# Performance work log

Measured on AMD Instinct MI355X. Metric: run time of the kernel, lower is better.

Reference implementation:

```python
import jax, jax.numpy as jnp
import numpy as np

N = 50000
E = 400000
R = 6
DIMS = (20, 256, 256, 512)


def setup_inputs() -> dict:
    key = jax.random.key(0)
    ks = jax.random.split(key, 16)
    inp = {
        "x": jax.random.normal(ks[0], (N, DIMS[0]), dtype=jnp.float32),
        "edge_index": jax.random.randint(ks[1], (2, E), 0, N, dtype=jnp.int64),
        "edge_type": jax.random.randint(ks[2], (E,), 0, R, dtype=jnp.int64),
    }
    # RGCN layer params: relation weights [R, in, out], root weight [in, out], bias [out]
    for li, (din, dout) in enumerate(zip(DIMS, DIMS[1:])):
        s = 1.0 / np.sqrt(din)
        inp[f"W{li}"] = jax.random.normal(ks[3 + 3 * li], (R, din, dout), dtype=jnp.float32) * s
        inp[f"root{li}"] = jax.random.normal(ks[4 + 3 * li], (din, dout), dtype=jnp.float32) * s
        inp[f"b{li}"] = jnp.zeros((dout,), dtype=jnp.float32)
    return inp


def _rgcn_layer(x, src, dst, etype, W, root, b):
    # Relation-specific transform of all nodes: [R, N, dout]
    h = jnp.einsum('ni,rio->rno', x, W)
    # Gather per-edge messages h[etype[e], src[e]] -> [E, dout]
    msgs = h[etype, src]
    # Mean-aggregate per (destination, relation) segment (PyG aggr='mean')
    seg = dst * R + etype  # [E]
    sums = jax.ops.segment_sum(msgs, seg, num_segments=N * R)          # [N*R, dout]
    cnt = jax.ops.segment_sum(jnp.ones((msgs.shape[0],), x.dtype), seg, num_segments=N * R)
    mean = sums / jnp.maximum(cnt, 1.0)[:, None]
    agg = mean.reshape(N, R, -1).sum(axis=1)  # sum over relations
    return agg + x @ root + b


def reference(x, edge_index, edge_type, W0, root0, b0, W1, root1, b1, W2, root2, b2):
    src, dst = edge_index[0], edge_index[1]  # messages flow source -> target
    params = ((W0, root0, b0), (W1, root1, b1), (W2, root2, b2))
    h = x
    for (W, root, b) in params:
        h = _rgcn_layer(h, src, dst, edge_type, W, root, b)
        h = jax.nn.relu(h)
    h = jnp.tanh(h)
    z = jnp.max(h, axis=0)          # graph-level max pool over nodes -> [latent]
    z = z / jnp.linalg.norm(z)      # normalized latent space
    return z[None, :]               # [1, latent]
```

## Files before the change

kernel.cpp:

```cpp
#include <hip/hip_runtime.h>

#define N_NODES 50000
#define N_EDGES 400000
#define N_REL 6
#define NSEG (N_NODES * N_REL)
#define NTILE ((N_NODES + 63) / 64)

#define SCAN_TILE 1024
#define SCAN_NB ((NSEG + SCAN_TILE - 1) / SCAN_TILE)

typedef float4 f4;
typedef short bf16x8 __attribute__((ext_vector_type(8)));
typedef float f32x4 __attribute__((ext_vector_type(4)));
typedef float f32x16 __attribute__((ext_vector_type(16)));
typedef int i32x8 __attribute__((ext_vector_type(8)));
typedef int i32x4 __attribute__((ext_vector_type(4)));

typedef __attribute__((address_space(1))) const void gvoid_t;
typedef __attribute__((address_space(3))) void lvoid_t;

__device__ __forceinline__ void gl_lds16(const void* g, void* l) {
    __builtin_amdgcn_global_load_lds((gvoid_t*)g, (lvoid_t*)l, 16, 0, 0);
}

__device__ __forceinline__ unsigned enc_f32(float f) {
    unsigned u = __float_as_uint(f);
    return (u & 0x80000000u) ? ~u : (u | 0x80000000u);
}
__device__ __forceinline__ float dec_f32(unsigned e) {
    return __uint_as_float((e & 0x80000000u) ? (e ^ 0x80000000u) : ~e);
}
__device__ __forceinline__ unsigned short bf16_rne(float x) {
    unsigned u = __float_as_uint(x);
    return (unsigned short)((u + 0x7FFFu + ((u >> 16) & 1u)) >> 16);
}
__device__ __forceinline__ unsigned fp8x4(float a0, float a1, float a2, float a3) {
    unsigned r = __builtin_amdgcn_cvt_pk_fp8_f32(a0, a1, 0, 0);
    r = __builtin_amdgcn_cvt_pk_fp8_f32(a2, a3, r, 1);
    return r;
}
__device__ __forceinline__ unsigned char fp8_1(float v) {
    return (unsigned char)(__builtin_amdgcn_cvt_pk_fp8_f32(v, v, 0, 0) & 0xFF);
}

#define SWZ(row, slot) ((size_t)(row) * 32 + (((slot) ^ (((row) >> 1) & 3)) * 8))

__global__ void count_seg(const int* __restrict__ ei, const int* __restrict__ et,
                          int* __restrict__ cnt) {
    int e = blockIdx.x * blockDim.x + threadIdx.x;
    if (e < N_EDGES) atomicAdd(&cnt[ei[N_EDGES + e] * N_REL + et[e]], 1);
}

__global__ void scan1(int* __restrict__ cnt, int* __restrict__ bsum) {
    __shared__ int sh[256];
    int t = threadIdx.x, b = blockIdx.x;
    int base = b * SCAN_TILE + t * 4;
    int v[4]; int s = 0;
    #pragma unroll
    for (int i = 0; i < 4; ++i) {
        v[i] = (base + i < NSEG) ? cnt[base + i] : 0;
        s += v[i];
    }
    sh[t] = s; __syncthreads();
    for (int o = 1; o < 256; o <<= 1) {
        int x = (t >= o) ? sh[t - o] : 0;
        __syncthreads();
        sh[t] += x;
        __syncthreads();
    }
    int run = sh[t] - s;
    #pragma unroll
    for (int i = 0; i < 4; ++i) {
        if (base + i < NSEG) cnt[base + i] = run;
        run += v[i];
    }
    if (t == 255) bsum[b] = sh[255];
}

__global__ void scan2(int* __restrict__ bsum) {
    __shared__ int sh[512];
    int t = threadIdx.x;
    int v = (t < SCAN_NB) ? bsum[t] : 0;
    sh[t] = v; __syncthreads();
    for (int o = 1; o < 512; o <<= 1) {
        int x = (t >= o) ? sh[t - o] : 0;
        __syncthreads();
        sh[t] += x;
        __syncthreads();
    }
    if (t < SCAN_NB) bsum[t] = sh[t] - v;
}

__global__ void scan3(const int* __restrict__ part, const int* __restrict__ bsum,
                      int* __restrict__ rowptr, int* __restrict__ fillptr) {
    int t = threadIdx.x, b = blockIdx.x;
    int base = b * SCAN_TILE + t * 4;
    int off = bsum[b];
    #pragma unroll
    for (int i = 0; i < 4; ++i) {
        if (base + i < NSEG) {
            int v = part[base + i] + off;
            rowptr[base + i] = v;
            fillptr[base + i] = v;
        }
    }
    if (b == 0 && t == 0) rowptr[NSEG] = N_EDGES;
}

__global__ void fill_edges(const int* __restrict__ ei, const int* __restrict__ et,
                           int* __restrict__ fillptr, int* __restrict__ esrc) {
    int e = blockIdx.x * blockDim.x + threadIdx.x;
    if (e < N_EDGES) {
        int seg = ei[N_EDGES + e] * N_REL + et[e];
        int p = atomicAdd(&fillptr[seg], 1);
        esrc[p] = ei[e];
    }
}

__global__ void rcp_kernel(const int* __restrict__ rowptr, float* __restrict__ rcp) {
    int s = blockIdx.x * blockDim.x + threadIdx.x;
    if (s < NSEG) {
        int c = rowptr[s + 1] - rowptr[s];
        rcp[s] = 1.0f / (float)(c > 1 ? c : 1);
    }
}

__global__ void prep_w0(const float* __restrict__ Wf, const float* __restrict__ rootW,
                        unsigned short* __restrict__ Wt,
                        int K1, int din, int dout, int KB) {
    int k = blockIdx.x;
    int n = blockIdx.y * 256 + threadIdx.x;
    if (n >= dout) return;
    float v = 0.f;
    if (k < K1) v = Wf[(size_t)k * dout + n];
    else if (k < K1 + din) v = rootW[(size_t)(k - K1) * dout + n];
    Wt[(size_t)n * KB + k] = bf16_rne(v);
}

__global__ void prep_wpk8(const float* __restrict__ Wf, const float* __restrict__ rootW,
                          unsigned char* __restrict__ Wpk, int K1, int dout) {
    int k = blockIdx.x;
    int ct = blockIdx.y;
    int nl = threadIdx.x;
    int col = ct * 256 + nl;
    float v = (k < K1) ? Wf[(size_t)k * dout + col]
                       : rootW[(size_t)(k - K1) * dout + col];
    v *= 16.0f;
    int p = k >> 6;
    Wpk[((size_t)(ct * 28 + p)) * 16384 + (size_t)nl * 64 + (k & 63)] = fp8_1(v);
}

__global__ void gather0(const float* __restrict__ x, const int* __restrict__ rowptr,
                        const int* __restrict__ esrc, const float* __restrict__ rcp,
                        unsigned short* __restrict__ Abf0) {
    int idx = blockIdx.x * blockDim.x + threadIdx.x;
    if (idx >= NSEG * 5) return;
    int s = idx / 5, q = idx - s * 5;
    float ax = 0.f, ay = 0.f, az = 0.f, aw = 0.f;
    int e0 = rowptr[s], e1 = rowptr[s + 1];
    for (int e = e0; e < e1; ++e) {
        const f4 u = *(const f4*)&x[(size_t)esrc[e] * 20 + q * 4];
        ax += u.x; ay += u.y; az += u.z; aw += u.w;
    }
    float sc = rcp[s];
    int node = s / N_REL, rel = s - node * N_REL;
    unsigned short* p = &Abf0[(size_t)node * 160 + rel * 20 + q * 4];
    unsigned o0 = bf16_rne(ax * sc) | ((unsigned)bf16_rne(ay * sc) << 16);
    unsigned o1 = bf16_rne(az * sc) | ((unsigned)bf16_rne(aw * sc) << 16);
    *(unsigned*)(p + 0) = o0;
    *(unsigned*)(p + 2) = o1;
}

__global__ void copyx0(const float* __restrict__ x, unsigned short* __restrict__ Abf0) {
    int t = blockIdx.x * blockDim.x + threadIdx.x;
    int n = t >> 5, d = t & 31;
    if (n >= N_NODES || d >= 20) return;
    Abf0[(size_t)n * 160 + 120 + d] = bf16_rne(x[(size_t)n * 20 + d]);
}

__global__ void gather_all8(const unsigned char* __restrict__ h8, const int* __restrict__ rowptr,
                            const int* __restrict__ esrc, const float* __restrict__ rcp,
                            unsigned char* __restrict__ Apk) {
    int t = blockIdx.x * blockDim.x + threadIdx.x;
    int sl = t >> 3;
    int q = t & 7;
    if (sl < NSEG) {
        int e0 = rowptr[sl], e1 = rowptr[sl + 1];
        float a[32];
        #pragma unroll
        for (int i = 0; i < 32; ++i) a[i] = 0.f;
        for (int e = e0; e < e1; ++e) {
            const unsigned char* hp = &h8[(size_t)esrc[e] * 256 + q * 32];
            #pragma unroll
            for (int c = 0; c < 2; ++c) {
                int4 v = *(const int4*)&hp[c * 16];
                const unsigned* pu = (const unsigned*)&v;
                #pragma unroll
                for (int j = 0; j < 4; ++j) {
                    unsigned u = pu[j];
                    a[c * 16 + j * 4 + 0] += __builtin_amdgcn_cvt_f32_fp8(u, 0);
                    a[c * 16 + j * 4 + 1] += __builtin_amdgcn_cvt_f32_fp8(u, 1);
                    a[c * 16 + j * 4 + 2] += __builtin_amdgcn_cvt_f32_fp8(u, 2);
                    a[c * 16 + j * 4 + 3] += __builtin_amdgcn_cvt_f32_fp8(u, 3);
                }
            }
        }
        float sc = rcp[sl];
        int node = sl / 6, rel = sl - node * 6;
        int rt = node >> 6, m = node & 63;
        int ks = rel * 8 + q;
        unsigned ow[8];
        #pragma unroll
        for (int i = 0; i < 8; ++i)
            ow[i] = fp8x4(a[4 * i] * sc, a[4 * i + 1] * sc, a[4 * i + 2] * sc, a[4 * i + 3] * sc);
        int p = ks >> 1, sp = ks & 1;
        unsigned char* dst = Apk + ((size_t)(rt * 28 + p)) * 4096 + (size_t)m * 64;
        int rot = (m >> 1) & 3;
        *(int4*)(dst + (((sp * 2 + 0 + rot) & 3) * 16)) = make_int4(ow[0], ow[1], ow[2], ow[3]);
        *(int4*)(dst + (((sp * 2 + 1 + rot) & 3) * 16)) = make_int4(ow[4], ow[5], ow[6], ow[7]);
    } else if (sl < NSEG + N_NODES) {
        int node = sl - NSEG;
        int rt = node >> 6, m = node & 63;
        const unsigned char* hp = &h8[(size_t)node * 256 + q * 32];
        int4 lo = *(const int4*)(hp + 0);
        int4 hi = *(const int4*)(hp + 16);
        int ks = 48 + q;
        int p = ks >> 1, sp = ks & 1;
        unsigned char* dst = Apk + ((size_t)(rt * 28 + p)) * 4096 + (size_t)m * 64;
        int rot = (m >> 1) & 3;
        *(int4*)(dst + (((sp * 2 + 0 + rot) & 3) * 16)) = lo;
        *(int4*)(dst + (((sp * 2 + 1 + rot) & 3) * 16)) = hi;
    }
}

__global__ __launch_bounds__(256)
void gemm_l0(const unsigned short* __restrict__ A, const unsigned short* __restrict__ Wt,
             const float* __restrict__ bias, unsigned char* __restrict__ outH8,
             int Ktot, int KB, int dout) {
    __shared__ unsigned short As[64 * 32];
    __shared__ unsigned short Bs[256 * 32];
    const int tid = threadIdx.x;
    const int col0 = blockIdx.x * 256;
    const int row0 = blockIdx.y * 64;
    const int w = tid >> 6, l = tid & 63;
    f32x4 acc[4][4] = {};

    for (int k0 = 0; k0 < Ktot; k0 += 32) {
        {
            int m = tid >> 2, slot = tid & 3;
            int4 v = {0, 0, 0, 0};
            int mg = row0 + m;
            if (mg < N_NODES) v = *(const int4*)&A[(size_t)mg * Ktot + k0 + slot * 8];
            *(int4*)&As[SWZ(m, slot)] = v;
        }
        {
            int nb = tid >> 2, slot = tid & 3;
            #pragma unroll
            for (int j = 0; j < 4; ++j) {
                int n = nb + j * 64;
                int4 v = *(const int4*)&Wt[(size_t)(col0 + n) * KB + k0 + slot * 8];
                *(int4*)&Bs[SWZ(n, slot)] = v;
            }
        }
        __syncthreads();
        bf16x8 af[4], bfr[4];
        #pragma unroll
        for (int rf = 0; rf < 4; ++rf)
            af[rf] = *(const bf16x8*)&As[SWZ(rf * 16 + (l & 15), l >> 4)];
        #pragma unroll
        for (int cf = 0; cf < 4; ++cf)
            bfr[cf] = *(const bf16x8*)&Bs[SWZ(w * 64 + cf * 16 + (l & 15), l >> 4)];
        #pragma unroll
        for (int cf = 0; cf < 4; ++cf)
            #pragma unroll
            for (int rf = 0; rf < 4; ++rf)
                acc[rf][cf] = __builtin_amdgcn_mfma_f32_16x16x32_bf16(
                    af[rf], bfr[cf], acc[rf][cf], 0, 0, 0);
        __syncthreads();
    }

    const int colbase = col0 + w * 64;
    #pragma unroll
    for (int cf = 0; cf < 4; ++cf) {
        int c = colbase + cf * 16 + (l & 15);
        float bb = bias[c];
        #pragma unroll
        for (int rf = 0; rf < 4; ++rf)
            #pragma unroll
            for (int i = 0; i < 4; ++i) {
                int m = row0 + rf * 16 + (l >> 4) * 4 + i;
                if (m < N_NODES) {
                    float v = fmaxf(acc[rf][cf][i] + bb, 0.f);
                    outH8[(size_t)m * dout + c] = fp8_1(v);
                }
            }
    }
}

__global__ __launch_bounds__(256, 3)
void gemm_mx(const unsigned char* __restrict__ Apk, const unsigned char* __restrict__ Wpk,
             const float* __restrict__ bias, unsigned char* __restrict__ outH8,
             unsigned* __restrict__ maxbuf, int dout, int fuse) {
    __shared__ __align__(16) unsigned char As[3][16384];
    __shared__ unsigned lmax[256];

    const int tid = threadIdx.x;
    const int w = tid >> 6, l = tid & 63;
    const int row0 = blockIdx.y * 64;
    const int bcol = blockIdx.x * 256;
    const int cg0 = bcol + w * 64;
    const int ctIdx = cg0 >> 8;
    const int nOff = cg0 & 255;

    f32x16 acc[2][2] = {};
    i32x8 aF[2];
    i32x4 bq[2][4];

    const unsigned char* aBlock = Apk + (size_t)blockIdx.y * 28 * 4096;
    const unsigned char* bLane = Wpk + (size_t)ctIdx * 28 * 16384
                               + (size_t)(nOff + (l & 31)) * 64 + (size_t)(l >> 5) * 32;

#define SB() __builtin_amdgcn_sched_barrier(0)

#define STAGE(g, buf) do {                                                   \
        _Pragma("unroll")                                                    \
        for (int i = 0; i < 4; ++i) {                                        \
            int c = w * 4 + i;                                               \
            gl_lds16(aBlock + (size_t)(g) * 16384 + (size_t)c * 1024 + l * 16, \
                     &As[buf][c * 1024]);                                    \
        }                                                                    \
    } while (0)

#define LOADB(p, s) do {                                                     \
        const unsigned char* _bp = bLane + (size_t)(p) * 16384;              \
        asm volatile("global_load_dwordx4 %0, %1, off"                       \
                     : "=&v"(bq[s][0]) : "v"(_bp));                          \
        asm volatile("global_load_dwordx4 %0, %1, off offset:16"             \
                     : "=&v"(bq[s][1]) : "v"(_bp));                          \
        asm volatile("global_load_dwordx4 %0, %1, off offset:2048"           \
                     : "=&v"(bq[s][2]) : "v"(_bp));                          \
        asm volatile("global_load_dwordx4 %0, %1, off offset:2064"           \
                     : "=&v"(bq[s][3]) : "v"(_bp));                          \
    } while (0)

#define READA(buf, q) do {                                                   \
        _Pragma("unroll")                                                    \
        for (int rf = 0; rf < 2; ++rf) {                                     \
            int mrow = rf * 32 + (l & 31);                                   \
            int rot = (mrow >> 1) & 3;                                       \
            int g = (l >> 5) * 2;                                            \
            const unsigned char* base = &As[buf][(q) * 4096 + (size_t)mrow * 64]; \
            i32x4 lo = *(const i32x4*)(base + (((g + 0 + rot) & 3) * 16));   \
            i32x4 hi = *(const i32x4*)(base + (((g + 1 + rot) & 3) * 16));   \
            i32x8 r;                                                         \
            r[0] = lo[0]; r[1] = lo[1]; r[2] = lo[2]; r[3] = lo[3];          \
            r[4] = hi[0]; r[5] = hi[1]; r[6] = hi[2]; r[7] = hi[3];          \
            aF[rf] = r;                                                      \
        }                                                                    \
    } while (0)

#define DOMFMA(s) do {                                                       \
        i32x8 Bq0, Bq1;                                                      \
        Bq0[0] = bq[s][0][0]; Bq0[1] = bq[s][0][1];                          \
        Bq0[2] = bq[s][0][2]; Bq0[3] = bq[s][0][3];                          \
        Bq0[4] = bq[s][1][0]; Bq0[5] = bq[s][1][1];                          \
        Bq0[6] = bq[s][1][2]; Bq0[7] = bq[s][1][3];                          \
        Bq1[0] = bq[s][2][0]; Bq1[1] = bq[s][2][1];                          \
        Bq1[2] = bq[s][2][2]; Bq1[3] = bq[s][2][3];                          \
        Bq1[4] = bq[s][3][0]; Bq1[5] = bq[s][3][1];                          \
        Bq1[6] = bq[s][3][2]; Bq1[7] = bq[s][3][3];                          \
        acc[0][0] = __builtin_amdgcn_mfma_scale_f32_32x32x64_f8f6f4(         \
            aF[0], Bq0, acc[0][0], 0, 0, 0, 127, 0, 123);                    \
        acc[1][0] = __builtin_amdgcn_mfma_scale_f32_32x32x64_f8f6f4(         \
            aF[1], Bq0, acc[1][0], 0, 0, 0, 127, 0, 123);                    \
        acc[0][1] = __builtin_amdgcn_mfma_scale_f32_32x32x64_f8f6f4(         \
            aF[0], Bq1, acc[0][1], 0, 0, 0, 127, 0, 123);                    \
        acc[1][1] = __builtin_amdgcn_mfma_scale_f32_32x32x64_f8f6f4(         \
            aF[1], Bq1, acc[1][1], 0, 0, 0, 127, 0, 123);                    \
    } while (0)

#define PHASE(buf, q, s, WN, p) do {                                         \
        READA(buf, q);                                                       \
        asm volatile("s_waitcnt vmcnt(" WN ")");                             \
        SB();                                                                \
        __builtin_amdgcn_s_setprio(1);                                       \
        DOMFMA(s);                                                           \
        __builtin_amdgcn_s_setprio(0);                                       \
        SB();                                                                \
        LOADB(p, s);                                                         \
        SB();                                                                \
    } while (0)

#define SSTEP(S, TW) do {                                                    \
        asm volatile("s_waitcnt vmcnt(" TW ")");                             \
        SB();                                                                \
        __builtin_amdgcn_s_barrier();                                        \
        SB();                                                                \
        PHASE((S) % 3, 0, 0, "8", 4 * (S) + 2 <= 27 ? 4 * (S) + 2 : 27);     \
        PHASE((S) % 3, 1, 1, "8", 4 * (S) + 3 <= 27 ? 4 * (S) + 3 : 27);     \
        PHASE((S) % 3, 2, 0, "4", 4 * (S) + 4 <= 27 ? 4 * (S) + 4 : 27);     \
        PHASE((S) % 3, 3, 1, "4", 4 * (S) + 5 <= 27 ? 4 * (S) + 5 : 27);     \
        STAGE((S) + 2 <= 6 ? (S) + 2 : 6, ((S) + 2) % 3);                    \
        SB();                                                                \
    } while (0)

    STAGE(0, 0);
    SB();
    LOADB(0, 0);
    LOADB(1, 1);
    SB();
    STAGE(1, 1);
    SB();

    SSTEP(0, "12");
    SSTEP(1, "20");
    SSTEP(2, "20");
    SSTEP(3, "20");
    SSTEP(4, "20");
    SSTEP(5, "20");
    SSTEP(6, "20");

#undef SSTEP
#undef PHASE
#undef DOMFMA
#undef READA
#undef LOADB
#undef STAGE
#undef SB

    if (!fuse) {
        #pragma unroll
        for (int cf = 0; cf < 2; ++cf) {
            int c = cg0 + cf * 32 + (l & 31);
            float bb = bias[c];
            #pragma unroll
            for (int rf = 0; rf < 2; ++rf)
                #pragma unroll
                for (int reg = 0; reg < 16; ++reg) {
                    int m = row0 + rf * 32 + (reg & 3) + 8 * (reg >> 2) + 4 * (l >> 5);
                    if (m < N_NODES) {
                        float v = fmaxf(acc[rf][cf][reg] + bb, 0.f);
                        outH8[(size_t)m * dout + c] = fp8_1(v);
                    }
                }
        }
    } else {
        lmax[tid] = 0u;
        __syncthreads();
        #pragma unroll
        for (int cf = 0; cf < 2; ++cf) {
            int c = cg0 + cf * 32 + (l & 31);
            float bb = bias[c];
            float mv = 0.f;
            bool any = false;
            #pragma unroll
            for (int rf = 0; rf < 2; ++rf)
                #pragma unroll
                for (int reg = 0; reg < 16; ++reg) {
                    int m = row0 + rf * 32 + (reg & 3) + 8 * (reg >> 2) + 4 * (l >> 5);
                    if (m < N_NODES) {
                        float v = acc[rf][cf][reg] + bb;
                        mv = any ? fmaxf(mv, v) : v;
                        any = true;
                    }
                }
            if (any) atomicMax(&lmax[c - bcol], enc_f32(mv));
        }
        __syncthreads();
        atomicMax(&maxbuf[bcol + tid], lmax[tid]);
    }
}

__global__ void finalize_kernel(const unsigned* __restrict__ maxbuf,
                                float* __restrict__ out) {
    __shared__ float red[8];
    int c = threadIdx.x;
    float v = dec_f32(maxbuf[c]);
    v = fmaxf(v, 0.0f);
    float t = tanhf(v);
    float s = t * t;
    #pragma unroll
    for (int o = 32; o > 0; o >>= 1) s += __shfl_down(s, o);
    int wid = c >> 6;
    if ((c & 63) == 0) red[wid] = s;
    __syncthreads();
    if (c < 8) {
        float wsum = red[c];
        #pragma unroll
        for (int o = 4; o > 0; o >>= 1) wsum += __shfl_down(wsum, o);
        if (c == 0) red[0] = wsum;
    }
    __syncthreads();
    float norm = sqrtf(red[0]);
    out[c] = t / norm;
}

static inline size_t align_up(size_t v, size_t a) { return (v + a - 1) / a * a; }

extern "C" void kernel_launch(void* const* d_in, const int* in_sizes, int n_in,
                              void* d_out, int out_size, void* d_ws, size_t ws_size,
                              hipStream_t stream) {
    const float* x  = (const float*)d_in[0];
    const int*   ei = (const int*)d_in[1];
    const int*   et = (const int*)d_in[2];
    const float* W0 = (const float*)d_in[3];
    const float* r0 = (const float*)d_in[4];
    const float* b0 = (const float*)d_in[5];
    const float* W1 = (const float*)d_in[6];
    const float* r1 = (const float*)d_in[7];
    const float* b1 = (const float*)d_in[8];
    const float* W2 = (const float*)d_in[9];
    const float* r2 = (const float*)d_in[10];
    const float* b2 = (const float*)d_in[11];
    float* out = (float*)d_out;

    char* ws = (char*)d_ws;
    size_t off = 0;
    int* cntpart = (int*)(ws + off); off = align_up(off + (size_t)NSEG * 4, 256);
    int* bsum = (int*)(ws + off);    off = align_up(off + 512 * 4, 256);
    int* rowptr = (int*)(ws + off);  off = align_up(off + (size_t)(NSEG + 1) * 4, 256);
    int* fillptr = (int*)(ws + off); off = align_up(off + (size_t)NSEG * 4, 256);
    int* esrc = (int*)(ws + off);    off = align_up(off + (size_t)N_EDGES * 4, 256);
    float* rcp = (float*)(ws + off); off = align_up(off + (size_t)NSEG * 4, 256);
    unsigned* maxbuf = (unsigned*)(ws + off); off = align_up(off + 512 * 4, 256);
    unsigned short* Wt0 = (unsigned short*)(ws + off); off = align_up(off + (size_t)256 * 160 * 2, 256);
    unsigned char* Wpk1 = (unsigned char*)(ws + off); off = align_up(off + (size_t)1 * 28 * 16384, 256);
    unsigned char* Wpk2 = (unsigned char*)(ws + off); off = align_up(off + (size_t)2 * 28 * 16384, 256);
    unsigned char* hbuf1 = (unsigned char*)(ws + off); off = align_up(off + (size_t)N_NODES * 256, 256);
    unsigned char* hbuf2 = (unsigned char*)(ws + off); off = align_up(off + (size_t)N_NODES * 256, 256);
    unsigned short* Abf0 = (unsigned short*)(ws + off); off = align_up(off + (size_t)N_NODES * 160 * 2, 256);
    unsigned char* Apk = (unsigned char*)(ws + off); off = align_up(off + (size_t)NTILE * 28 * 4096, 256);
    if (ws_size < off) return;

    hipMemsetAsync(cntpart, 0, (size_t)NSEG * 4, stream);
    count_seg<<<(N_EDGES + 255) / 256, 256, 0, stream>>>(ei, et, cntpart);
    scan1<<<SCAN_NB, 256, 0, stream>>>(cntpart, bsum);
    scan2<<<1, 512, 0, stream>>>(bsum);
    scan3<<<SCAN_NB, 256, 0, stream>>>(cntpart, bsum, rowptr, fillptr);
    rcp_kernel<<<(NSEG + 255) / 256, 256, 0, stream>>>(rowptr, rcp);
    fill_edges<<<(N_EDGES + 255) / 256, 256, 0, stream>>>(ei, et, fillptr, esrc);
    hipMemsetAsync(maxbuf, 0, 512 * 4, stream);

    prep_w0<<<dim3(160, 1), 256, 0, stream>>>(W0, r0, Wt0, 120, 20, 256, 160);
    prep_wpk8<<<dim3(1792, 1), 256, 0, stream>>>(W1, r1, Wpk1, 1536, 256);
    prep_wpk8<<<dim3(1792, 2), 256, 0, stream>>>(W2, r2, Wpk2, 1536, 512);

    hipMemsetAsync(Abf0, 0, (size_t)N_NODES * 160 * 2, stream);
    gather0<<<(NSEG * 5 + 255) / 256, 256, 0, stream>>>(x, rowptr, esrc, rcp, Abf0);
    copyx0<<<(N_NODES * 32 + 255) / 256, 256, 0, stream>>>(x, Abf0);
    gemm_l0<<<dim3(1, NTILE), 256, 0, stream>>>(Abf0, Wt0, b0, hbuf1, 160, 160, 256);

    const int gthreads = (NSEG + N_NODES) * 8;

    gather_all8<<<(gthreads + 255) / 256, 256, 0, stream>>>(hbuf1, rowptr, esrc, rcp, Apk);
    gemm_mx<<<dim3(1, NTILE), 256, 0, stream>>>(Apk, Wpk1, b1, hbuf2, nullptr, 256, 0);

    gather_all8<<<(gthreads + 255) / 256, 256, 0, stream>>>(hbuf2, rowptr, esrc, rcp, Apk);
    gemm_mx<<<dim3(2, NTILE), 256, 0, stream>>>(Apk, Wpk2, b2, nullptr, maxbuf, 512, 1);

    finalize_kernel<<<1, 512, 0, stream>>>(maxbuf, out);
}
```

Measured before the change: 308.3 us.

## Halve gemm_mx row tile to 32 rows and rebuild the staging pipeline

The MX-fp8 GEMM now gives each block 32 rows instead of 64, so twice as many blocks are launched, each with a smaller LDS footprint and half the accumulators. Occupancy is raised to 4 blocks per CU. The A staging, LDS reads and software pipeline are reworked into 14 half-steps with new vmcnt waits. In exchange, each B (weight) fragment is reused across only 32 rows, so weight traffic from global/L2 doubles, and MFMA density per B load drops.

After: 351.3 us. 1.14x slower.

```diff
diff --git a/kernel.cpp b/kernel.cpp
--- a/kernel.cpp
+++ b/kernel.cpp
@@ -5,6 +5,7 @@
 #define N_REL 6
 #define NSEG (N_NODES * N_REL)
 #define NTILE ((N_NODES + 63) / 64)
+#define NTILE32 (2 * NTILE)
 
 #define SCAN_TILE 1024
 #define SCAN_NB ((NSEG + SCAN_TILE - 1) / SCAN_TILE)
@@ -297,39 +298,36 @@
     }
 }
 
-__global__ __launch_bounds__(256, 3)
+__global__ __launch_bounds__(256, 4)
 void gemm_mx(const unsigned char* __restrict__ Apk, const unsigned char* __restrict__ Wpk,
              const float* __restrict__ bias, unsigned char* __restrict__ outH8,
              unsigned* __restrict__ maxbuf, int dout, int fuse) {
-    __shared__ __align__(16) unsigned char As[3][16384];
+    __shared__ __align__(16) unsigned char As[3][4096];
     __shared__ unsigned lmax[256];
 
     const int tid = threadIdx.x;
     const int w = tid >> 6, l = tid & 63;
-    const int row0 = blockIdx.y * 64;
+    const int row0 = blockIdx.y * 32;
+    const int rt = blockIdx.y >> 1;
+    const int half = blockIdx.y & 1;
     const int bcol = blockIdx.x * 256;
     const int cg0 = bcol + w * 64;
     const int ctIdx = cg0 >> 8;
     const int nOff = cg0 & 255;
 
-    f32x16 acc[2][2] = {};
-    i32x8 aF[2];
+    f32x16 acc[2] = {};
+    i32x8 aF;
     i32x4 bq[2][4];
 
-    const unsigned char* aBlock = Apk + (size_t)blockIdx.y * 28 * 4096;
+    const unsigned char* sSrc = Apk + (size_t)rt * 28 * 4096
+                              + (size_t)(w >> 1) * 4096 + (size_t)half * 2048
+                              + (size_t)(w & 1) * 1024 + (size_t)l * 16;
     const unsigned char* bLane = Wpk + (size_t)ctIdx * 28 * 16384
                                + (size_t)(nOff + (l & 31)) * 64 + (size_t)(l >> 5) * 32;
 
 #define SB() __builtin_amdgcn_sched_barrier(0)
 
-#define STAGE(g, buf) do {                                                   \
-        _Pragma("unroll")                                                    \
-        for (int i = 0; i < 4; ++i) {                                        \
-            int c = w * 4 + i;                                               \
-            gl_lds16(aBlock + (size_t)(g) * 16384 + (size_t)c * 1024 + l * 16, \
-                     &As[buf][c * 1024]);                                    \
-        }                                                                    \
-    } while (0)
+#define STAGE(g, buf) gl_lds16(sSrc + (size_t)(g) * 8192, &As[buf][w * 1024])
 
 #define LOADB(p, s) do {                                                     \
         const unsigned char* _bp = bLane + (size_t)(p) * 16384;              \
@@ -344,19 +342,16 @@
     } while (0)
 
 #define READA(buf, q) do {                                                   \
-        _Pragma("unroll")                                                    \
-        for (int rf = 0; rf < 2; ++rf) {                                     \
-            int mrow = rf * 32 + (l & 31);                                   \
-            int rot = (mrow >> 1) & 3;                                       \
-            int g = (l >> 5) * 2;                                            \
-            const unsigned char* base = &As[buf][(q) * 4096 + (size_t)mrow * 64]; \
-            i32x4 lo = *(const i32x4*)(base + (((g + 0 + rot) & 3) * 16));   \
-            i32x4 hi = *(const i32x4*)(base + (((g + 1 + rot) & 3) * 16));   \
-            i32x8 r;                                                         \
-            r[0] = lo[0]; r[1] = lo[1]; r[2] = lo[2]; r[3] = lo[3];          \
-            r[4] = hi[0]; r[5] = hi[1]; r[6] = hi[2]; r[7] = hi[3];          \
-            aF[rf] = r;                                                      \
-        }                                                                    \
+        int rr = l & 31;                                                     \
+        int rot = (l >> 1) & 3;                                              \
+        int g = (l >> 5) * 2;                                                \
+        const unsigned char* base = &As[buf][(q) * 2048 + (size_t)rr * 64];  \
+        i32x4 lo = *(const i32x4*)(base + (((g + 0 + rot) & 3) * 16));       \
+        i32x4 hi = *(const i32x4*)(base + (((g + 1 + rot) & 3) * 16));       \
+        i32x8 r;                                                             \
+        r[0] = lo[0]; r[1] = lo[1]; r[2] = lo[2]; r[3] = lo[3];              \
+        r[4] = hi[0]; r[5] = hi[1]; r[6] = hi[2]; r[7] = hi[3];              \
+        aF = r;                                                              \
     } while (0)
 
 #define DOMFMA(s) do {                                                       \
@@ -369,19 +364,15 @@
         Bq1[2] = bq[s][2][2]; Bq1[3] = bq[s][2][3];                          \
         Bq1[4] = bq[s][3][0]; Bq1[5] = bq[s][3][1];                          \
         Bq1[6] = bq[s][3][2]; Bq1[7] = bq[s][3][3];                          \
-        acc[0][0] = __builtin_amdgcn_mfma_scale_f32_32x32x64_f8f6f4(         \
-            aF[0], Bq0, acc[0][0], 0, 0, 0, 127, 0, 123);                    \
-        acc[1][0] = __builtin_amdgcn_mfma_scale_f32_32x32x64_f8f6f4(         \
-            aF[1], Bq0, acc[1][0], 0, 0, 0, 127, 0, 123);                    \
-        acc[0][1] = __builtin_amdgcn_mfma_scale_f32_32x32x64_f8f6f4(         \
-            aF[0], Bq1, acc[0][1], 0, 0, 0, 127, 0, 123);                    \
-        acc[1][1] = __builtin_amdgcn_mfma_scale_f32_32x32x64_f8f6f4(         \
-            aF[1], Bq1, acc[1][1], 0, 0, 0, 127, 0, 123);                    \
+        acc[0] = __builtin_amdgcn_mfma_scale_f32_32x32x64_f8f6f4(            \
+            aF, Bq0, acc[0], 0, 0, 0, 127, 0, 123);                          \
+        acc[1] = __builtin_amdgcn_mfma_scale_f32_32x32x64_f8f6f4(            \
+            aF, Bq1, acc[1], 0, 0, 0, 127, 0, 123);                          \
     } while (0)
 
-#define PHASE(buf, q, s, WN, p) do {                                         \
+#define PHASE(buf, q, s, p) do {                                             \
         READA(buf, q);                                                       \
-        asm volatile("s_waitcnt vmcnt(" WN ")");                             \
+        asm volatile("s_waitcnt vmcnt(5)");                                  \
         SB();                                                                \
         __builtin_amdgcn_s_setprio(1);                                       \
         DOMFMA(s);                                                           \
@@ -391,16 +382,14 @@
         SB();                                                                \
     } while (0)
 
-#define SSTEP(S, TW) do {                                                    \
-        asm volatile("s_waitcnt vmcnt(" TW ")");                             \
+#define HSTEP(H) do {                                                        \
+        asm volatile("s_waitcnt vmcnt(9)");                                  \
         SB();                                                                \
         __builtin_amdgcn_s_barrier();                                        \
         SB();                                                                \
-        PHASE((S) % 3, 0, 0, "8", 4 * (S) + 2 <= 27 ? 4 * (S) + 2 : 27);     \
-        PHASE((S) % 3, 1, 1, "8", 4 * (S) + 3 <= 27 ? 4 * (S) + 3 : 27);     \
-        PHASE((S) % 3, 2, 0, "4", 4 * (S) + 4 <= 27 ? 4 * (S) + 4 : 27);     \
-        PHASE((S) % 3, 3, 1, "4", 4 * (S) + 5 <= 27 ? 4 * (S) + 5 : 27);     \
-        STAGE((S) + 2 <= 6 ? (S) + 2 : 6, ((S) + 2) % 3);                    \
+        PHASE((H) % 3, 0, 0, 2 * (H) + 2 <= 27 ? 2 * (H) + 2 : 27);          \
+        PHASE((H) % 3, 1, 1, 2 * (H) + 3 <= 27 ? 2 * (H) + 3 : 27);          \
+        STAGE((H) + 2 <= 13 ? (H) + 2 : 13, ((H) + 2) % 3);                  \
         SB();                                                                \
     } while (0)
 
@@ -412,15 +401,16 @@
     STAGE(1, 1);
     SB();
 
-    SSTEP(0, "12");
-    SSTEP(1, "20");
-    SSTEP(2, "20");
-    SSTEP(3, "20");
-    SSTEP(4, "20");
-    SSTEP(5, "20");
-    SSTEP(6, "20");
-
-#undef SSTEP
+    HSTEP(0);  HSTEP(1);  HSTEP(2);  HSTEP(3);
+    HSTEP(4);  HSTEP(5);  HSTEP(6);  HSTEP(7);
+    HSTEP(8);  HSTEP(9);  HSTEP(10); HSTEP(11);
+    HSTEP(12); HSTEP(13);
+
+    SB();
+    asm volatile("s_waitcnt vmcnt(0)");
+    SB();
+
+#undef HSTEP
 #undef PHASE
 #undef DOMFMA
 #undef READA
@@ -434,15 +424,13 @@
             int c = cg0 + cf * 32 + (l & 31);
             float bb = bias[c];
             #pragma unroll
-            for (int rf = 0; rf < 2; ++rf)
-                #pragma unroll
-                for (int reg = 0; reg < 16; ++reg) {
-                    int m = row0 + rf * 32 + (reg & 3) + 8 * (reg >> 2) + 4 * (l >> 5);
-                    if (m < N_NODES) {
-                        float v = fmaxf(acc[rf][cf][reg] + bb, 0.f);
-                        outH8[(size_t)m * dout + c] = fp8_1(v);
-                    }
+            for (int reg = 0; reg < 16; ++reg) {
+                int m = row0 + (reg & 3) + 8 * (reg >> 2) + 4 * (l >> 5);
+                if (m < N_NODES) {
+                    float v = fmaxf(acc[cf][reg] + bb, 0.f);
+                    outH8[(size_t)m * dout + c] = fp8_1(v);
                 }
+            }
         }
     } else {
         lmax[tid] = 0u;
@@ -454,16 +442,14 @@
             float mv = 0.f;
             bool any = false;
             #pragma unroll
-            for (int rf = 0; rf < 2; ++rf)
-                #pragma unroll
-                for (int reg = 0; reg < 16; ++reg) {
-                    int m = row0 + rf * 32 + (reg & 3) + 8 * (reg >> 2) + 4 * (l >> 5);
-                    if (m < N_NODES) {
-                        float v = acc[rf][cf][reg] + bb;
-                        mv = any ? fmaxf(mv, v) : v;
-                        any = true;
-                    }
+            for (int reg = 0; reg < 16; ++reg) {
+                int m = row0 + (reg & 3) + 8 * (reg >> 2) + 4 * (l >> 5);
+                if (m < N_NODES) {
+                    float v = acc[cf][reg] + bb;
+                    mv = any ? fmaxf(mv, v) : v;
+                    any = true;
                 }
+            }
             if (any) atomicMax(&lmax[c - bcol], enc_f32(mv));
         }
         __syncthreads();
@@ -553,10 +539,10 @@
     const int gthreads = (NSEG + N_NODES) * 8;
 
     gather_all8<<<(gthreads + 255) / 256, 256, 0, stream>>>(hbuf1, rowptr, esrc, rcp, Apk);
-    gemm_mx<<<dim3(1, NTILE), 256, 0, stream>>>(Apk, Wpk1, b1, hbuf2, nullptr, 256, 0);
+    gemm_mx<<<dim3(1, NTILE32), 256, 0, stream>>>(Apk, Wpk1, b1, hbuf2, nullptr, 256, 0);
 
     gather_all8<<<(gthreads + 255) / 256, 256, 0, stream>>>(hbuf2, rowptr, esrc, rcp, Apk);
-    gemm_mx<<<dim3(2, NTILE), 256, 0, stream>>>(Apk, Wpk2, b2, nullptr, maxbuf, 512, 1);
+    gemm_mx<<<dim3(2, NTILE32), 256, 0, stream>>>(Apk, Wpk2, b2, nullptr, maxbuf, 512, 1);
 
     finalize_kernel<<<1, 512, 0, stream>>>(maxbuf, out);
 }
```
